# Optimization experiments

Measured on AMD Instinct MI355X. Metric: run time of the kernel, lower is better.

The kernel has to match this reference:

```python
import jax, jax.numpy as jnp
import numpy as np

B, S, D, H = 2, 2048, 2048, 16
HD = D // H  # 128


def setup_inputs() -> dict:
    key = jax.random.key(0)
    ks = jax.random.split(key, 6)
    sc = 0.02
    return {
        "x": jax.random.normal(ks[0], (B, S, D), jnp.float32),
        "attention_mask": jnp.ones((B, S), jnp.int32),
        "w_qkv": jax.random.normal(ks[1], (D, 3 * D), jnp.float32) * sc,
        "b_qkv": jnp.zeros((3 * D,), jnp.float32),
        "w_o": jax.random.normal(ks[2], (D, D), jnp.float32) * sc,
        "b_o": jnp.zeros((D,), jnp.float32),
        "ln1_w": jnp.ones((D,), jnp.float32),
        "w1": jax.random.normal(ks[3], (D, 8 * D), jnp.float32) * sc,
        "b1": jnp.zeros((8 * D,), jnp.float32),
        "w2": jax.random.normal(ks[4], (4 * D, D), jnp.float32) * sc,
        "b2": jnp.zeros((D,), jnp.float32),
        "ln2_w": jnp.ones((D,), jnp.float32),
    }


def rmsnorm(x, w, eps=1e-6):
    rms = jnp.sqrt(jnp.mean(x * x, axis=-1, keepdims=True) + eps)
    return w * (x / rms)


def rope_tables(seq_len, dim, base=10000.0):
    inv_freq = 1.0 / (base ** (jnp.arange(0, dim, 2, dtype=jnp.float32) / dim))
    t = jnp.arange(seq_len, dtype=jnp.float32)
    freqs = t[:, None] * inv_freq[None, :]          # [S, dim/2]
    emb = jnp.concatenate([freqs, freqs], axis=-1)  # [S, dim]
    return jnp.cos(emb), jnp.sin(emb)


def apply_rope(x, cos, sin):
    # Faithful to source: rotate pairs, then out = rot*cos + roll(rot,1)*sin
    xr = x.reshape(*x.shape[:-1], -1, 2)
    x1, x2 = xr[..., 0], xr[..., 1]
    rot = jnp.stack([-x2, x1], axis=-1).reshape(x.shape)
    return rot * cos + jnp.roll(rot, shift=1, axis=-1) * sin


def transformer_layer(x, attention_mask, w_qkv, b_qkv, w_o, b_o, ln1_w, w1, b1, w2, b2, ln2_w):
    residual = x
    qkv = x @ w_qkv + b_qkv                         # [B,S,3D]
    q, k, v = jnp.split(qkv, 3, axis=-1)
    split = lambda t: t.reshape(B, S, H, HD).transpose(0, 2, 1, 3)  # [B,H,S,HD]
    q, k, v = split(q), split(k), split(v)

    cos, sin = rope_tables(S, HD)                   # [S,HD], broadcasts over B,H
    q = apply_rope(q, cos, sin)
    k = apply_rope(k, cos, sin)

    scores = jnp.einsum("bhqd,bhkd->bhqk", q, k) / jnp.sqrt(jnp.float32(HD))
    mask = (attention_mask == 1)[:, None, None, :]  # [B,1,1,S]
    scores = jnp.where(mask, scores, -jnp.inf)
    attn = jax.nn.softmax(scores, axis=-1)
    out = jnp.einsum("bhqk,bhkd->bhqd", attn, v)
    out = out.transpose(0, 2, 1, 3).reshape(B, S, D)
    out = out @ w_o + b_o

    x = rmsnorm(out + residual, ln1_w)
    residual = x
    h = x @ w1 + b1                                 # [B,S,8D]
    h, gate = jnp.split(h, 2, axis=-1)
    h = h * jax.nn.gelu(gate, approximate=False)
    h = h @ w2 + b2
    return rmsnorm(h + residual, ln2_w)


def reference(x, attention_mask, w_qkv, b_qkv, w_o, b_o, ln1_w, w1, b1, w2, b2, ln2_w):
    return transformer_layer(x, attention_mask, w_qkv, b_qkv, w_o, b_o, ln1_w, w1, b1, w2, b2, ln2_w)
```

## Files before the change

kernel.cpp:

```cpp
#include <hip/hip_runtime.h>
#include <cstdint>

typedef unsigned short u16;
typedef __attribute__((ext_vector_type(8))) short short8;
typedef __attribute__((ext_vector_type(8))) unsigned short ushortx8;
typedef __attribute__((ext_vector_type(4))) float floatx4;

#define DEV __device__ __forceinline__

DEV u16 f2bf(float f) {
  union { float f; uint32_t u; } x; x.f = f;
  uint32_t r = x.u + 0x7fffu + ((x.u >> 16) & 1u);
  return (u16)(r >> 16);
}
DEV float bf2f(u16 h) {
  union { float f; uint32_t u; } x; x.u = ((uint32_t)h) << 16;
  return x.f;
}
DEV float fast_gelu(float g) {
  float u = 0.7978845608f * (g + 0.044715f * g * g * g);
  float e = __expf(-2.0f * fabsf(u));
  float th = (1.0f - e) / (1.0f + e);
  th = (u < 0.0f) ? -th : th;
  return 0.5f * g * (1.0f + th);
}
DEV void gload_lds16(const void* g, void* lds) {
  __builtin_amdgcn_global_load_lds(
      (const __attribute__((address_space(1))) char*)(uintptr_t)g,
      (__attribute__((address_space(3))) char*)(uintptr_t)lds, 16, 0, 0);
}


__global__ __launch_bounds__(256) void k_cvt_bf16(const float* __restrict__ in,
                                                  u16* __restrict__ out, int n) {
  int i = (blockIdx.x * 256 + threadIdx.x) * 8;
  if (i + 7 < n) {
    float4 a = *(const float4*)(in + i);
    float4 b = *(const float4*)(in + i + 4);
    ushortx8 o;
    o[0] = f2bf(a.x); o[1] = f2bf(a.y); o[2] = f2bf(a.z); o[3] = f2bf(a.w);
    o[4] = f2bf(b.x); o[5] = f2bf(b.y); o[6] = f2bf(b.z); o[7] = f2bf(b.w);
    *(ushortx8*)(out + i) = o;
  }
}

__global__ __launch_bounds__(256) void k_transpose_all(const float* __restrict__ Wq,
                                                       u16* __restrict__ WqT,
                                                       const float* __restrict__ Wo,
                                                       u16* __restrict__ WoT,
                                                       const float* __restrict__ W2,
                                                       u16* __restrict__ W2T) {
  __shared__ u16 t[64][70];
  int id = blockIdx.x;
  const float* W; u16* Wt; int R, C, tix;
  if (id < 3072)      { W = Wq; Wt = WqT; R = 2048; C = 6144; tix = id; }
  else if (id < 4096) { W = Wo; Wt = WoT; R = 2048; C = 2048; tix = id - 3072; }
  else                { W = W2; Wt = W2T; R = 8192; C = 2048; tix = id - 4096; }
  int ntc = C >> 6;
  int c0 = (tix % ntc) * 64, r0 = (tix / ntc) * 64;
  int cx = threadIdx.x & 15, ry = threadIdx.x >> 4;
#pragma unroll
  for (int i = 0; i < 4; ++i) {
    int row = ry + i * 16;
    float4 v = *(const float4*)(W + (size_t)(r0 + row) * C + c0 + cx * 4);
    ushort2 lo, hi;
    lo.x = f2bf(v.x); lo.y = f2bf(v.y);
    hi.x = f2bf(v.z); hi.y = f2bf(v.w);
    *(ushort2*)&t[row][cx * 4] = lo;
    *(ushort2*)&t[row][cx * 4 + 2] = hi;
  }
  __syncthreads();
#pragma unroll
  for (int i = 0; i < 4; ++i) {
    int col = ry + i * 16;
    ushort4 o;
    o.x = t[cx * 4 + 0][col]; o.y = t[cx * 4 + 1][col];
    o.z = t[cx * 4 + 2][col]; o.w = t[cx * 4 + 3][col];
    *(ushort4*)(Wt + (size_t)(c0 + col) * R + r0 + cx * 4) = o;
  }
}

__global__ __launch_bounds__(256) void k_transpose_w1p(const float* __restrict__ W,
                                                       u16* __restrict__ Wt) {
  __shared__ u16 t[64][70];
  int c0 = blockIdx.x * 64;
  int r0 = blockIdx.y * 64;
  int cx = threadIdx.x & 15, ry = threadIdx.x >> 4;
  int eta = c0 + cx * 4;
  int Bq = eta >> 8, ii = eta & 255, wn = (ii >> 6) & 3, rr = ii & 63, n = rr >> 4, tt = rr & 15;
  int src = Bq * 128 + wn * 32 + (n & 1) * 16 + tt + ((n >= 2) ? 8192 : 0);
#pragma unroll
  for (int i = 0; i < 4; ++i) {
    int row = ry + i * 16;
    float4 v = *(const float4*)(W + (size_t)(r0 + row) * 16384 + src);
    ushort2 lo, hi;
    lo.x = f2bf(v.x); lo.y = f2bf(v.y);
    hi.x = f2bf(v.z); hi.y = f2bf(v.w);
    *(ushort2*)&t[row][cx * 4] = lo;
    *(ushort2*)&t[row][cx * 4 + 2] = hi;
  }
  __syncthreads();
#pragma unroll
  for (int i = 0; i < 4; ++i) {
    ushort4 o;
    int col = ry + i * 16;
    o.x = t[cx * 4 + 0][col]; o.y = t[cx * 4 + 1][col];
    o.z = t[cx * 4 + 2][col]; o.w = t[cx * 4 + 3][col];
    *(ushort4*)(Wt + (size_t)(c0 + col) * 2048 + r0 + cx * 4) = o;
  }
}

__global__ __launch_bounds__(256) void k_rope_tab(float* __restrict__ ct, float* __restrict__ st) {
  int i = blockIdx.x * 256 + threadIdx.x;
  int s = i >> 6, j = i & 63;
  float invf = 1.0f / powf(10000.0f, (float)j * (1.0f / 64.0f));
  float ang = (float)s * invf;
  ct[i] = cosf(ang);
  st[i] = sinf(ang);
}

template <int EPI>
__global__ __launch_bounds__(512, 2) void k_gemm256(const u16* __restrict__ A,
                                                    const u16* __restrict__ Bt,
                                                    void* __restrict__ C,
                                                    const float* __restrict__ bias,
                                                    int M, int N, int K, int nsplit,
                                                    u16* __restrict__ qrO,
                                                    u16* __restrict__ krO,
                                                    u16* __restrict__ vtO,
                                                    const float* __restrict__ ctabO,
                                                    const float* __restrict__ stabO) {
  __shared__ __align__(16) u16 lds[4][2][8192];
  const int tid = threadIdx.x;
  const int w = tid >> 6, lane = tid & 63;
  const int l15 = lane & 15, l4 = lane >> 4;
  const int wm = w >> 2, wn = w & 3;
  const int nbn = N >> 8;
  const int nbm = M >> 8;

  int bm, bn, split = 0;
  if (nsplit == 1 && nbm == 16 && (nbn & 7) == 0) {
    const int xcd = blockIdx.x & 7, l = blockIdx.x >> 3;
    const int xr = xcd >> 1, xc = xcd & 1;
    const int stn = l >> 4, lbm = (l >> 2) & 3, lbn = l & 3;
    bm = xr * 4 + lbm;
    bn = xc * (nbn >> 1) + stn * 4 + lbn;
  } else {
    const int nwg = gridDim.x;
    const int q = nwg >> 3, r8 = nwg & 7;
    const int xcd = blockIdx.x & 7, loc = blockIdx.x >> 3;
    const int swz = (xcd < r8 ? xcd * (q + 1) : r8 * (q + 1) + (xcd - r8) * q) + loc;
    const int ntiles = nwg / nsplit;
    split = swz / ntiles;
    const int tix = swz % ntiles;
    bm = tix / nbn; bn = tix % nbn;
  }
  const int klen = K / nsplit;
  const int kofs = split * klen;

  const size_t abase = (size_t)bm * 256 * K + kofs;
  const size_t bbase = (size_t)bn * 256 * K + kofs;
  const int nt = klen >> 5;

  const int sr = tid >> 2;
  const int sc = (tid & 3) ^ ((sr >> 1) & 3);
  auto stage = [&](int kt, int li, int op) {
    const u16* src = op ? (Bt + bbase) : (A + abase);
    gload_lds16(src + (size_t)(li * 128 + sr) * K + kt * 32 + sc * 8,
                (void*)&lds[kt & 3][op][(li * 512 + w * 64) * 8]);
  };

  const int fro = l15 * 32 + (l4 ^ ((l15 >> 1) & 3)) * 8;

  floatx4 acc[8][4];
  floatx4 zero = {0.f, 0.f, 0.f, 0.f};
#pragma unroll
  for (int m = 0; m < 8; ++m)
#pragma unroll
    for (int n = 0; n < 4; ++n) acc[m][n] = zero;

  for (int kt = 0; kt < 3; ++kt)
    if (kt < nt) {
      stage(kt, 0, 0); stage(kt, 0, 1);
      stage(kt, 1, 0); stage(kt, 1, 1);
    }

  for (int t = 0; t < nt; ++t) {
    const int buf = t & 3;
    if (t < nt - 2)       asm volatile("s_waitcnt vmcnt(8)" ::: "memory");
    else if (t == nt - 2) asm volatile("s_waitcnt vmcnt(4)" ::: "memory");
    else                  asm volatile("s_waitcnt vmcnt(0)" ::: "memory");
    __builtin_amdgcn_sched_barrier(0);
    __builtin_amdgcn_s_barrier();
    const u16* Ab = &lds[buf][0][wm * 4096 + fro];
    const u16* Bb = &lds[buf][1][wn * 2048 + fro];
    short8 av[4], bv[4];
#pragma unroll
    for (int n = 0; n < 4; ++n) bv[n] = *(const short8*)(Bb + n * 512);
#pragma unroll
    for (int i = 0; i < 4; ++i) av[i] = *(const short8*)(Ab + i * 512);
    if (t + 3 < nt) { stage(t + 3, 0, 0); stage(t + 3, 0, 1); }
    asm volatile("s_waitcnt lgkmcnt(0)" ::: "memory");
    __builtin_amdgcn_sched_barrier(0);
    __builtin_amdgcn_s_setprio(1);
#pragma unroll
    for (int i = 0; i < 4; ++i)
#pragma unroll
      for (int n = 0; n < 4; ++n)
        acc[i][n] = __builtin_amdgcn_mfma_f32_16x16x32_bf16(av[i], bv[n], acc[i][n], 0, 0, 0);
    __builtin_amdgcn_s_setprio(0);
    __builtin_amdgcn_s_barrier();
#pragma unroll
    for (int i = 0; i < 4; ++i) av[i] = *(const short8*)(Ab + (4 + i) * 512);
    if (t + 3 < nt) { stage(t + 3, 1, 0); stage(t + 3, 1, 1); }
    asm volatile("s_waitcnt lgkmcnt(0)" ::: "memory");
    __builtin_amdgcn_sched_barrier(0);
    __builtin_amdgcn_s_setprio(1);
#pragma unroll
    for (int i = 0; i < 4; ++i)
#pragma unroll
      for (int n = 0; n < 4; ++n)
        acc[4 + i][n] = __builtin_amdgcn_mfma_f32_16x16x32_bf16(av[i], bv[n], acc[4 + i][n], 0, 0, 0);
    __builtin_amdgcn_s_setprio(0);
  }

  const int row0 = bm * 256 + wm * 128, col0 = bn * 256 + wn * 64;
  if (EPI == 2) {
    float* P = (float*)C + (size_t)split * M * N;
#pragma unroll
    for (int n = 0; n < 4; ++n) {
      int col = col0 + n * 16 + l15;
#pragma unroll
      for (int m = 0; m < 8; ++m)
#pragma unroll
        for (int j = 0; j < 4; ++j) {
          int row = row0 + m * 16 + l4 * 4 + j;
          P[(size_t)row * N + col] = acc[m][n][j];
        }
    }
  } else if (EPI == 3) {
    __syncthreads();
    u16* ep = ((u16*)lds) + w * 4096;
    const int colA = bn * 128 + wn * 32;
#pragma unroll
    for (int n = 0; n < 2; ++n) {
      float ba = bias[colA + n * 16 + l15];
      float bg = bias[8192 + colA + n * 16 + l15];
#pragma unroll
      for (int m = 0; m < 8; ++m)
#pragma unroll
        for (int j = 0; j < 4; ++j) {
          float a = acc[m][n][j] + ba;
          float g = acc[m][n + 2][j] + bg;
          ep[(m * 16 + l4 * 4 + j) * 32 + n * 16 + l15] = f2bf(a * fast_gelu(g));
        }
    }
    const int rr = lane >> 2, cg = lane & 3;
    u16* Cg = (u16*)C;
    const int Nact = N >> 1;
#pragma unroll
    for (int pass = 0; pass < 8; ++pass) {
      short8 v = *(const short8*)&ep[(pass * 16 + rr) * 32 + cg * 8];
      size_t grow = row0 + pass * 16 + rr;
      *(short8*)&Cg[grow * Nact + colA + cg * 8] = v;
    }
  } else if (EPI == 4) {
    constexpr int PAD = 264;
    u16* T = (u16*)lds;
    const int bq = bm >> 3;
    const int srow0 = (bm & 7) * 256;
#pragma unroll 1
    for (int hf = 0; hf < 2; ++hf) {
      __syncthreads();
      if (wm == hf) {
#pragma unroll
        for (int n = 0; n < 4; ++n) {
          float bb = bias[bn * 256 + wn * 64 + n * 16 + l15];
#pragma unroll
          for (int m = 0; m < 8; ++m)
#pragma unroll
            for (int j = 0; j < 4; ++j)
              T[(m * 16 + l4 * 4 + j) * PAD + wn * 64 + n * 16 + l15] =
                  f2bf(acc[m][n][j] + bb);
        }
      }
      __syncthreads();
      if (bn < 16) {
        int sl = tid >> 2, hh = (tid >> 1) & 1, t2 = tid & 1;
        const u16* row = T + sl * PAD + hh * 128;
        int s = srow0 + hf * 128 + sl;
        int head = 2 * (bn & 7) + hh;
        u16* dst = (bn < 8 ? qrO : krO) +
                   (((size_t)bq * 16 + head) * 2048 + s) * 128 + t2 * 64;
        const float* ctr = ctabO + (s << 6);
        const float* str2 = stabO + (s << 6);
#pragma unroll
        for (int ch = 0; ch < 8; ++ch) {
          int d0 = t2 * 64 + ch * 8;
          ushortx8 xv = *(const ushortx8*)(row + d0);
          float xp = bf2f(row[(d0 + 126) & 127]);
          int f0 = d0 & 63;
          float4 c0v = *(const float4*)(ctr + f0);
          float4 c1v = *(const float4*)(ctr + f0 + 4);
          float4 s0v = *(const float4*)(str2 + f0);
          float4 s1v = *(const float4*)(str2 + f0 + 4);
          float cc[8] = {c0v.x, c0v.y, c0v.z, c0v.w, c1v.x, c1v.y, c1v.z, c1v.w};
          float sn[8] = {s0v.x, s0v.y, s0v.z, s0v.w, s1v.x, s1v.y, s1v.z, s1v.w};
          ushortx8 o;
#pragma unroll
          for (int pr = 0; pr < 4; ++pr) {
            float xe = bf2f((u16)xv[2 * pr]), xo = bf2f((u16)xv[2 * pr + 1]);
            o[2 * pr]     = f2bf(-xo * cc[2 * pr] + xp * sn[2 * pr]);
            o[2 * pr + 1] = f2bf( xe * cc[2 * pr + 1] - xo * sn[2 * pr + 1]);
            xp = xe;
          }
          *(ushortx8*)(dst + ch * 8) = o;
        }
      } else {
        int hh = tid >> 8, dg = (tid >> 4) & 15, sc2 = tid & 15;
        int head = 2 * (bn - 16) + hh;
        int s0 = srow0 + hf * 128 + sc2 * 8;
        ushortx8 r[8];
#pragma unroll
        for (int i = 0; i < 8; ++i)
          r[i] = *(const ushortx8*)(T + (sc2 * 8 + i) * PAD + hh * 128 + dg * 8);
        u16* vbase = vtO + ((size_t)bq * 2048 + head * 128 + dg * 8) * 2048 + s0;
#pragma unroll
        for (int j2 = 0; j2 < 8; ++j2) {
          ushortx8 o;
#pragma unroll
          for (int i = 0; i < 8; ++i) o[i] = r[i][j2];
          *(ushortx8*)(vbase + (size_t)j2 * 2048) = o;
        }
      }
    }
  } else {
    __syncthreads();
    u16* ep = ((u16*)lds) + w * 8192;
#pragma unroll
    for (int n = 0; n < 4; ++n) {
      float bb = bias[col0 + n * 16 + l15];
#pragma unroll
      for (int m = 0; m < 8; ++m)
#pragma unroll
        for (int j = 0; j < 4; ++j)
          ep[(m * 16 + l4 * 4 + j) * 64 + n * 16 + l15] = f2bf(acc[m][n][j] + bb);
    }
    const int rr = lane >> 3, cg = lane & 7;
    u16* Cg = (u16*)C;
#pragma unroll
    for (int pass = 0; pass < 16; ++pass) {
      short8 v = *(const short8*)&ep[(pass * 8 + rr) * 64 + cg * 8];
      size_t grow = row0 + pass * 8 + rr;
      *(short8*)&Cg[grow * N + col0 + cg * 8] = v;
    }
  }
}

__global__ __launch_bounds__(512, 4) void k_attn(const u16* __restrict__ Qr,
                                                 const u16* __restrict__ Kr,
                                                 const u16* __restrict__ Vt,
                                                 const int* __restrict__ mask,
                                                 u16* __restrict__ O) {
  constexpr int S = 2048, HD = 128, H = 16;
  __shared__ __align__(16) u16 Ksh[64 * 128];
  __shared__ __align__(16) u16 Vsh[128 * 64];
  __shared__ __align__(16) u16 Psh[8][16 * 72];
  __shared__ float Msh[2048];

  const int bid = blockIdx.x;
  const int xcd = bid & 7, local = bid >> 3;
  const int bh = xcd * 4 + (local >> 4);
  const int qt = local & 15;
  const int b = bh >> 4, h = bh & 15;
  const int tid = threadIdx.x, wave = tid >> 6, lane = tid & 63;
  const int l15 = lane & 15, l4 = lane >> 4;
  const size_t bhs = (size_t)(b * H + h);
  const u16* Qb = Qr + bhs * S * HD;
  const u16* Kb = Kr + bhs * S * HD;
  const u16* Vb = Vt + bhs * HD * S;

  for (int i = tid; i < 2048; i += 512)
    Msh[i] = (mask[b * S + i] == 1) ? 0.0f : -1e30f;

  const int qrow = qt * 128 + wave * 16 + l15;
  short8 qf[4];
#pragma unroll
  for (int kk = 0; kk < 4; ++kk)
    qf[kk] = *(const short8*)&Qb[(size_t)qrow * HD + kk * 32 + l4 * 8];

  const int giA = tid, giB = 512 + tid;
  const int rKA = giA >> 4, gKA = giA & 15;
  const int rKB = giB >> 4, gKB = giB & 15;
  const int gsKA = (gKA & 8) | ((gKA ^ rKA) & 7);
  const int gsKB = (gKB & 8) | ((gKB ^ rKB) & 7);
  const int rVA = giA >> 3, gVA = giA & 7;
  const int rVB = giB >> 3, gVB = giB & 7;
  const int gsVA = (gVA ^ rVA) & 7;
  const int gsVB = (gVB ^ rVB) & 7;
  const u16* pKA = Kb + (size_t)rKA * HD + gsKA * 8;
  const u16* pKB = Kb + (size_t)rKB * HD + gsKB * 8;
  const u16* pVA = Vb + (size_t)rVA * S + gsVA * 8;
  const u16* pVB = Vb + (size_t)rVB * S + gsVB * 8;

  float m_run[4], l_run[4];
  floatx4 o_acc[8];
  floatx4 zero = {0.f, 0.f, 0.f, 0.f};
#pragma unroll
  for (int j = 0; j < 4; ++j) { m_run[j] = -1e30f; l_run[j] = 0.f; }
#pragma unroll
  for (int n = 0; n < 8; ++n) o_acc[n] = zero;

  uint4 k0 = *(const uint4*)pKA;
  uint4 k1 = *(const uint4*)pKB;
  uint4 v0 = *(const uint4*)pVA;
  uint4 v1 = *(const uint4*)pVB;

  for (int ktile = 0; ktile < S / 64; ++ktile) {
    __builtin_amdgcn_sched_barrier(0);
    __builtin_amdgcn_s_barrier();
    __builtin_amdgcn_sched_barrier(0);
    *(uint4*)&Ksh[(size_t)(0 * 512 + tid) * 8] = k0;
    *(uint4*)&Ksh[(size_t)(1 * 512 + tid) * 8] = k1;
    *(uint4*)&Vsh[(size_t)(0 * 512 + tid) * 8] = v0;
    *(uint4*)&Vsh[(size_t)(1 * 512 + tid) * 8] = v1;
    if (ktile + 1 < S / 64) {
      k0 = *(const uint4*)(pKA + (size_t)(ktile + 1) * 8192);
      k1 = *(const uint4*)(pKB + (size_t)(ktile + 1) * 8192);
      v0 = *(const uint4*)(pVA + (size_t)(ktile + 1) * 64);
      v1 = *(const uint4*)(pVB + (size_t)(ktile + 1) * 64);
    }
    asm volatile("s_waitcnt lgkmcnt(0)" ::: "memory");
    __builtin_amdgcn_sched_barrier(0);
    __builtin_amdgcn_s_barrier();
    __builtin_amdgcn_sched_barrier(0);

    floatx4 s_acc[4];
#pragma unroll
    for (int nf = 0; nf < 4; ++nf) s_acc[nf] = zero;
    __builtin_amdgcn_s_setprio(1);
#pragma unroll
    for (int kk = 0; kk < 4; ++kk) {
#pragma unroll
      for (int nf = 0; nf < 4; ++nf) {
        int key = nf * 16 + l15;
        int G = kk * 4 + l4;
        int lg = (G & 8) | ((G ^ key) & 7);
        short8 kv = *(const short8*)&Ksh[key * 128 + lg * 8];
        s_acc[nf] = __builtin_amdgcn_mfma_f32_16x16x32_bf16(qf[kk], kv, s_acc[nf], 0, 0, 0);
      }
    }
    __builtin_amdgcn_s_setprio(0);

    const float scale = 0.08838834764831845f;
    float p[4][4];
#pragma unroll
    for (int nf = 0; nf < 4; ++nf) {
      float ma = Msh[ktile * 64 + nf * 16 + l15];
#pragma unroll
      for (int j = 0; j < 4; ++j) p[nf][j] = s_acc[nf][j] * scale + ma;
    }
#pragma unroll
    for (int j = 0; j < 4; ++j) {
      float mx = fmaxf(fmaxf(p[0][j], p[1][j]), fmaxf(p[2][j], p[3][j]));
      mx = fmaxf(mx, __shfl_xor(mx, 1));
      mx = fmaxf(mx, __shfl_xor(mx, 2));
      mx = fmaxf(mx, __shfl_xor(mx, 4));
      mx = fmaxf(mx, __shfl_xor(mx, 8));
      float mnew = fmaxf(m_run[j], mx);
      float corr = __expf(m_run[j] - mnew);
      float ps = 0.f;
#pragma unroll
      for (int nf = 0; nf < 4; ++nf) {
        p[nf][j] = __expf(p[nf][j] - mnew);
        ps += p[nf][j];
      }
      l_run[j] = l_run[j] * corr + ps;
      m_run[j] = mnew;
#pragma unroll
      for (int n = 0; n < 8; ++n) o_acc[n][j] *= corr;
    }

#pragma unroll
    for (int nf = 0; nf < 4; ++nf)
#pragma unroll
      for (int j = 0; j < 4; ++j)
        Psh[wave][(l4 * 4 + j) * 72 + nf * 16 + l15] = f2bf(p[nf][j]);

    __builtin_amdgcn_s_setprio(1);
#pragma unroll
    for (int ks = 0; ks < 2; ++ks) {
      short8 pa = *(const short8*)&Psh[wave][l15 * 72 + ks * 32 + l4 * 8];
#pragma unroll
      for (int nf2 = 0; nf2 < 8; ++nf2) {
        int hd = nf2 * 16 + l15;
        int G = ks * 4 + l4;
        short8 vv = *(const short8*)&Vsh[hd * 64 + ((G ^ hd) & 7) * 8];
        o_acc[nf2] = __builtin_amdgcn_mfma_f32_16x16x32_bf16(pa, vv, o_acc[nf2], 0, 0, 0);
      }
    }
    __builtin_amdgcn_s_setprio(0);
  }

#pragma unroll
  for (int j = 0; j < 4; ++j) {
    float ls = l_run[j];
    ls += __shfl_xor(ls, 1); ls += __shfl_xor(ls, 2);
    ls += __shfl_xor(ls, 4); ls += __shfl_xor(ls, 8);
    l_run[j] = ls;
  }

#pragma unroll
  for (int j = 0; j < 4; ++j) {
    float inv = 1.0f / l_run[j];
    int srow = qt * 128 + wave * 16 + l4 * 4 + j;
    size_t orow = ((size_t)b * S + srow) * 2048 + h * 128;
#pragma unroll
    for (int nf2 = 0; nf2 < 8; ++nf2)
      O[orow + nf2 * 16 + l15] = f2bf(o_acc[nf2][j] * inv);
  }
}

__global__ __launch_bounds__(256) void k_rms_fuse1(const float* __restrict__ p0,
                                                   const float* __restrict__ p1,
                                                   const float* __restrict__ bias,
                                                   const float* __restrict__ resid,
                                                   const float* __restrict__ w,
                                                   u16* __restrict__ ob) {
  int row = blockIdx.x;
  int t = threadIdx.x;
  size_t base = (size_t)row * 2048 + t * 8;
  float4 a0 = *(const float4*)(p0 + base);
  float4 a1 = *(const float4*)(p0 + base + 4);
  float4 b0 = *(const float4*)(p1 + base);
  float4 b1 = *(const float4*)(p1 + base + 4);
  float4 r0 = *(const float4*)(resid + base);
  float4 r1 = *(const float4*)(resid + base + 4);
  float4 c0 = *(const float4*)(bias + t * 8);
  float4 c1 = *(const float4*)(bias + t * 8 + 4);
  float v[8];
  v[0] = a0.x + b0.x + r0.x + c0.x; v[1] = a0.y + b0.y + r0.y + c0.y;
  v[2] = a0.z + b0.z + r0.z + c0.z; v[3] = a0.w + b0.w + r0.w + c0.w;
  v[4] = a1.x + b1.x + r1.x + c1.x; v[5] = a1.y + b1.y + r1.y + c1.y;
  v[6] = a1.z + b1.z + r1.z + c1.z; v[7] = a1.w + b1.w + r1.w + c1.w;
  float ss = 0.f;
#pragma unroll
  for (int e = 0; e < 8; ++e) ss += v[e] * v[e];
#pragma unroll
  for (int d = 1; d < 64; d <<= 1) ss += __shfl_xor(ss, d);
  __shared__ float sred[4];
  if ((t & 63) == 0) sred[t >> 6] = ss;
  __syncthreads();
  float tot = sred[0] + sred[1] + sred[2] + sred[3];
  float scale = rsqrtf(tot * (1.0f / 2048.0f) + 1e-6f);
  const float* wp = w + t * 8;
  ushort4 q0, q1;
  q0.x = f2bf(v[0] * wp[0] * scale); q0.y = f2bf(v[1] * wp[1] * scale);
  q0.z = f2bf(v[2] * wp[2] * scale); q0.w = f2bf(v[3] * wp[3] * scale);
  q1.x = f2bf(v[4] * wp[4] * scale); q1.y = f2bf(v[5] * wp[5] * scale);
  q1.z = f2bf(v[6] * wp[6] * scale); q1.w = f2bf(v[7] * wp[7] * scale);
  *(ushort4*)(ob + base) = q0;
  *(ushort4*)(ob + base + 4) = q1;
}

__global__ __launch_bounds__(256) void k_rms_fuse2(const float* __restrict__ p0,
                                                   const float* __restrict__ p1,
                                                   const float* __restrict__ bias,
                                                   const u16* __restrict__ residb,
                                                   const float* __restrict__ w,
                                                   float* __restrict__ of) {
  int row = blockIdx.x;
  int t = threadIdx.x;
  size_t base = (size_t)row * 2048 + t * 8;
  float4 a0 = *(const float4*)(p0 + base);
  float4 a1 = *(const float4*)(p0 + base + 4);
  float4 b0 = *(const float4*)(p1 + base);
  float4 b1 = *(const float4*)(p1 + base + 4);
  ushortx8 rb = *(const ushortx8*)(residb + base);
  float4 c0 = *(const float4*)(bias + t * 8);
  float4 c1 = *(const float4*)(bias + t * 8 + 4);
  float v[8];
  v[0] = a0.x + b0.x + c0.x; v[1] = a0.y + b0.y + c0.y;
  v[2] = a0.z + b0.z + c0.z; v[3] = a0.w + b0.w + c0.w;
  v[4] = a1.x + b1.x + c1.x; v[5] = a1.y + b1.y + c1.y;
  v[6] = a1.z + b1.z + c1.z; v[7] = a1.w + b1.w + c1.w;
#pragma unroll
  for (int e = 0; e < 8; ++e) v[e] += bf2f((u16)rb[e]);
  float ss = 0.f;
#pragma unroll
  for (int e = 0; e < 8; ++e) ss += v[e] * v[e];
#pragma unroll
  for (int d = 1; d < 64; d <<= 1) ss += __shfl_xor(ss, d);
  __shared__ float sred[4];
  if ((t & 63) == 0) sred[t >> 6] = ss;
  __syncthreads();
  float tot = sred[0] + sred[1] + sred[2] + sred[3];
  float scale = rsqrtf(tot * (1.0f / 2048.0f) + 1e-6f);
  const float* wp = w + t * 8;
  float4 f0, f1;
  f0.x = v[0] * wp[0] * scale; f0.y = v[1] * wp[1] * scale;
  f0.z = v[2] * wp[2] * scale; f0.w = v[3] * wp[3] * scale;
  f1.x = v[4] * wp[4] * scale; f1.y = v[5] * wp[5] * scale;
  f1.z = v[6] * wp[6] * scale; f1.w = v[7] * wp[7] * scale;
  *(float4*)(of + base) = f0;
  *(float4*)(of + base + 4) = f1;
}

extern "C" void kernel_launch(void* const* d_in, const int* in_sizes, int n_in,
                              void* d_out, int out_size, void* d_ws, size_t ws_size,
                              hipStream_t stream) {
  const float* x     = (const float*)d_in[0];
  const int*   amask = (const int*)d_in[1];
  const float* w_qkv = (const float*)d_in[2];
  const float* b_qkv = (const float*)d_in[3];
  const float* w_o   = (const float*)d_in[4];
  const float* b_o   = (const float*)d_in[5];
  const float* ln1_w = (const float*)d_in[6];
  const float* w1    = (const float*)d_in[7];
  const float* b1    = (const float*)d_in[8];
  const float* w2    = (const float*)d_in[9];
  const float* b2    = (const float*)d_in[10];
  const float* ln2_w = (const float*)d_in[11];
  float* out = (float*)d_out;

  char* ws = (char*)d_ws;
  u16*   xb    = (u16*)(ws + 0);
  u16*   wqkvT = (u16*)(ws + 16777216);
  u16*   woT   = (u16*)(ws + 41943040);
  u16*   w1Tp  = (u16*)(ws + 50331648);
  u16*   w2T   = (u16*)(ws + 117440512);
  float* ctab  = (float*)(ws + 150994944);
  float* stab  = (float*)(ws + 151519232);
  u16*   qr    = (u16*)(ws + 202375168);
  u16*   kr    = (u16*)(ws + 219152384);
  u16*   vt    = (u16*)(ws + 235929600);
  u16*   aout  = (u16*)(ws + 252706816);
  u16*   x1b   = (u16*)(ws + 303038464);
  float* p01a  = (float*)(ws + 152043520);
  u16*   act   = (u16*)(ws + 152043520);
  float* p01b  = (float*)(ws + 219152384);

  k_cvt_bf16<<<4096, 256, 0, stream>>>(x, xb, 4096 * 2048);
  k_transpose_all<<<8192, 256, 0, stream>>>(w_qkv, wqkvT, w_o, woT, w2, w2T);
  k_transpose_w1p<<<dim3(256, 32), 256, 0, stream>>>(w1, w1Tp);
  k_rope_tab<<<512, 256, 0, stream>>>(ctab, stab);

  k_gemm256<4><<<16 * 24, 512, 0, stream>>>(xb, wqkvT, nullptr, b_qkv,
                                            4096, 6144, 2048, 1,
                                            qr, kr, vt, ctab, stab);
  k_attn<<<512, 512, 0, stream>>>(qr, kr, vt, amask, aout);

  k_gemm256<2><<<16 * 8 * 2, 512, 0, stream>>>(aout, woT, p01a, nullptr,
                                               4096, 2048, 2048, 2,
                                               nullptr, nullptr, nullptr, nullptr, nullptr);
  k_rms_fuse1<<<4096, 256, 0, stream>>>(p01a, p01a + (size_t)4096 * 2048, b_o, x, ln1_w, x1b);

  k_gemm256<3><<<16 * 64, 512, 0, stream>>>(x1b, w1Tp, act, b1,
                                            4096, 16384, 2048, 1,
                                            nullptr, nullptr, nullptr, nullptr, nullptr);

  k_gemm256<2><<<16 * 8 * 2, 512, 0, stream>>>(act, w2T, p01b, nullptr,
                                               4096, 2048, 8192, 2,
                                               nullptr, nullptr, nullptr, nullptr, nullptr);
  k_rms_fuse2<<<4096, 256, 0, stream>>>(p01b, p01b + (size_t)4096 * 2048, b2, x1b, ln2_w, out);
}
```

Baseline: 832.1 us.

## Store split-K partials in fp16 and fold softmax scale into Q with exp2

Split-K GEMM partial outputs are written as fp16 instead of fp32, halving the write and read traffic between the out-projection and FFN-down GEMMs and the RMSNorm fuse kernels. The softmax scale times log2(e) is folded into Q during the RoPE epilogue, so attention uses exp2 directly and skips a multiply per score. GELU's exp is also switched to exp2. This trades some precision (fp16 partials can overflow or lose bits, and Q is stored pre-scaled in bf16) for less memory traffic and fewer ALU ops.

```diff
diff --git a/kernel.cpp b/kernel.cpp
--- a/kernel.cpp
+++ b/kernel.cpp
@@ -1,5 +1,6 @@
 #include <hip/hip_runtime.h>
 #include <cstdint>
+#include <cstring>
 
 typedef unsigned short u16;
 typedef __attribute__((ext_vector_type(8))) short short8;
@@ -17,9 +18,16 @@
   union { float f; uint32_t u; } x; x.u = ((uint32_t)h) << 16;
   return x.f;
 }
+DEV u16 f2h(float f) {
+  union { u16 u; _Float16 h; } x; x.h = (_Float16)f; return x.u;
+}
+DEV float h2f(u16 h) {
+  union { u16 u; _Float16 h; } x; x.u = h; return (float)x.h;
+}
+DEV float fexp2(float x) { return __builtin_amdgcn_exp2f(x); }
 DEV float fast_gelu(float g) {
   float u = 0.7978845608f * (g + 0.044715f * g * g * g);
-  float e = __expf(-2.0f * fabsf(u));
+  float e = fexp2(-2.885390082f * fabsf(u));
   float th = (1.0f - e) / (1.0f + e);
   th = (u < 0.0f) ? -th : th;
   return 0.5f * g * (1.0f + th);
@@ -226,7 +234,7 @@
 
   const int row0 = bm * 256 + wm * 128, col0 = bn * 256 + wn * 64;
   if (EPI == 2) {
-    float* P = (float*)C + (size_t)split * M * N;
+    u16* P = (u16*)C + (size_t)split * M * N;
 #pragma unroll
     for (int n = 0; n < 4; ++n) {
       int col = col0 + n * 16 + l15;
@@ -235,7 +243,7 @@
 #pragma unroll
         for (int j = 0; j < 4; ++j) {
           int row = row0 + m * 16 + l4 * 4 + j;
-          P[(size_t)row * N + col] = acc[m][n][j];
+          P[(size_t)row * N + col] = f2h(acc[m][n][j]);
         }
     }
   } else if (EPI == 3) {
@@ -294,6 +302,7 @@
                    (((size_t)bq * 16 + head) * 2048 + s) * 128 + t2 * 64;
         const float* ctr = ctabO + (s << 6);
         const float* str2 = stabO + (s << 6);
+        const float qs = (bn < 8) ? 0.12751744f : 1.0f;
 #pragma unroll
         for (int ch = 0; ch < 8; ++ch) {
           int d0 = t2 * 64 + ch * 8;
@@ -310,8 +319,8 @@
 #pragma unroll
           for (int pr = 0; pr < 4; ++pr) {
             float xe = bf2f((u16)xv[2 * pr]), xo = bf2f((u16)xv[2 * pr + 1]);
-            o[2 * pr]     = f2bf(-xo * cc[2 * pr] + xp * sn[2 * pr]);
-            o[2 * pr + 1] = f2bf( xe * cc[2 * pr + 1] - xo * sn[2 * pr + 1]);
+            o[2 * pr]     = f2bf((-xo * cc[2 * pr] + xp * sn[2 * pr]) * qs);
+            o[2 * pr + 1] = f2bf(( xe * cc[2 * pr + 1] - xo * sn[2 * pr + 1]) * qs);
             xp = xe;
           }
           *(ushortx8*)(dst + ch * 8) = o;
@@ -452,13 +461,12 @@
     }
     __builtin_amdgcn_s_setprio(0);
 
-    const float scale = 0.08838834764831845f;
     float p[4][4];
 #pragma unroll
     for (int nf = 0; nf < 4; ++nf) {
       float ma = Msh[ktile * 64 + nf * 16 + l15];
 #pragma unroll
-      for (int j = 0; j < 4; ++j) p[nf][j] = s_acc[nf][j] * scale + ma;
+      for (int j = 0; j < 4; ++j) p[nf][j] = s_acc[nf][j] + ma;
     }
 #pragma unroll
     for (int j = 0; j < 4; ++j) {
@@ -468,11 +476,11 @@
       mx = fmaxf(mx, __shfl_xor(mx, 4));
       mx = fmaxf(mx, __shfl_xor(mx, 8));
       float mnew = fmaxf(m_run[j], mx);
-      float corr = __expf(m_run[j] - mnew);
+      float corr = fexp2(m_run[j] - mnew);
       float ps = 0.f;
 #pragma unroll
       for (int nf = 0; nf < 4; ++nf) {
-        p[nf][j] = __expf(p[nf][j] - mnew);
+        p[nf][j] = fexp2(p[nf][j] - mnew);
         ps += p[nf][j];
       }
       l_run[j] = l_run[j] * corr + ps;
@@ -521,8 +529,8 @@
   }
 }
 
-__global__ __launch_bounds__(256) void k_rms_fuse1(const float* __restrict__ p0,
-                                                   const float* __restrict__ p1,
+__global__ __launch_bounds__(256) void k_rms_fuse1(const u16* __restrict__ p0,
+                                                   const u16* __restrict__ p1,
                                                    const float* __restrict__ bias,
                                                    const float* __restrict__ resid,
                                                    const float* __restrict__ w,
@@ -530,19 +538,18 @@
   int row = blockIdx.x;
   int t = threadIdx.x;
   size_t base = (size_t)row * 2048 + t * 8;
-  float4 a0 = *(const float4*)(p0 + base);
-  float4 a1 = *(const float4*)(p0 + base + 4);
-  float4 b0 = *(const float4*)(p1 + base);
-  float4 b1 = *(const float4*)(p1 + base + 4);
+  ushortx8 a = *(const ushortx8*)(p0 + base);
+  ushortx8 b = *(const ushortx8*)(p1 + base);
   float4 r0 = *(const float4*)(resid + base);
   float4 r1 = *(const float4*)(resid + base + 4);
   float4 c0 = *(const float4*)(bias + t * 8);
   float4 c1 = *(const float4*)(bias + t * 8 + 4);
+  float rr[8] = {r0.x, r0.y, r0.z, r0.w, r1.x, r1.y, r1.z, r1.w};
+  float cc[8] = {c0.x, c0.y, c0.z, c0.w, c1.x, c1.y, c1.z, c1.w};
   float v[8];
-  v[0] = a0.x + b0.x + r0.x + c0.x; v[1] = a0.y + b0.y + r0.y + c0.y;
-  v[2] = a0.z + b0.z + r0.z + c0.z; v[3] = a0.w + b0.w + r0.w + c0.w;
-  v[4] = a1.x + b1.x + r1.x + c1.x; v[5] = a1.y + b1.y + r1.y + c1.y;
-  v[6] = a1.z + b1.z + r1.z + c1.z; v[7] = a1.w + b1.w + r1.w + c1.w;
+#pragma unroll
+  for (int e = 0; e < 8; ++e)
+    v[e] = h2f((u16)a[e]) + h2f((u16)b[e]) + rr[e] + cc[e];
   float ss = 0.f;
 #pragma unroll
   for (int e = 0; e < 8; ++e) ss += v[e] * v[e];
@@ -563,8 +570,8 @@
   *(ushort4*)(ob + base + 4) = q1;
 }
 
-__global__ __launch_bounds__(256) void k_rms_fuse2(const float* __restrict__ p0,
-                                                   const float* __restrict__ p1,
+__global__ __launch_bounds__(256) void k_rms_fuse2(const u16* __restrict__ p0,
+                                                   const u16* __restrict__ p1,
                                                    const float* __restrict__ bias,
                                                    const u16* __restrict__ residb,
                                                    const float* __restrict__ w,
@@ -572,20 +579,16 @@
   int row = blockIdx.x;
   int t = threadIdx.x;
   size_t base = (size_t)row * 2048 + t * 8;
-  float4 a0 = *(const float4*)(p0 + base);
-  float4 a1 = *(const float4*)(p0 + base + 4);
-  float4 b0 = *(const float4*)(p1 + base);
-  float4 b1 = *(const float4*)(p1 + base + 4);
+  ushortx8 a = *(const ushortx8*)(p0 + base);
+  ushortx8 b = *(const ushortx8*)(p1 + base);
   ushortx8 rb = *(const ushortx8*)(residb + base);
   float4 c0 = *(const float4*)(bias + t * 8);
   float4 c1 = *(const float4*)(bias + t * 8 + 4);
+  float cc[8] = {c0.x, c0.y, c0.z, c0.w, c1.x, c1.y, c1.z, c1.w};
   float v[8];
-  v[0] = a0.x + b0.x + c0.x; v[1] = a0.y + b0.y + c0.y;
-  v[2] = a0.z + b0.z + c0.z; v[3] = a0.w + b0.w + c0.w;
-  v[4] = a1.x + b1.x + c1.x; v[5] = a1.y + b1.y + c1.y;
-  v[6] = a1.z + b1.z + c1.z; v[7] = a1.w + b1.w + c1.w;
-#pragma unroll
-  for (int e = 0; e < 8; ++e) v[e] += bf2f((u16)rb[e]);
+#pragma unroll
+  for (int e = 0; e < 8; ++e)
+    v[e] = h2f((u16)a[e]) + h2f((u16)b[e]) + bf2f((u16)rb[e]) + cc[e];
   float ss = 0.f;
 #pragma unroll
   for (int e = 0; e < 8; ++e) ss += v[e] * v[e];
@@ -636,9 +639,9 @@
   u16*   vt    = (u16*)(ws + 235929600);
   u16*   aout  = (u16*)(ws + 252706816);
   u16*   x1b   = (u16*)(ws + 303038464);
-  float* p01a  = (float*)(ws + 152043520);
+  u16*   p01a  = (u16*)(ws + 152043520);
   u16*   act   = (u16*)(ws + 152043520);
-  float* p01b  = (float*)(ws + 219152384);
+  u16*   p01b  = (u16*)(ws + 219152384);
 
   k_cvt_bf16<<<4096, 256, 0, stream>>>(x, xb, 4096 * 2048);
   k_transpose_all<<<8192, 256, 0, stream>>>(w_qkv, wqkvT, w_o, woT, w2, w2T);
```

New measurement: 817.5 us. No clear change (-1.7%).
